# Kernel tuning notes

Measured on AMD Instinct MI355X. Metric: run time of the kernel, lower is better.

Reference implementation:

```python
import jax, jax.numpy as jnp
import numpy as np

RANGE_DISP = 32
IND_INPUT_VIEW = np.array([1, 9]) - 1  # 0-based indices of the two input views
TOTAL_VIEWS = 9                         # an_sparse + an_novel
FEAT_CH = 64


def conv2d(x, w, b):
    # x: (N, Cin, H, W), w: (Cout, Cin, kh, kw), SAME padding, stride 1
    y = jax.lax.conv_general_dilated(x, w, (1, 1), 'SAME',
                                     dimension_numbers=('NCHW', 'OIHW', 'NCHW'))
    return y + b[None, :, None, None]


def unfold_1xK(x, K):
    # torch.nn.functional.unfold(x, kernel_size=(1, K)) for x: (M, C, H, W)
    # -> (M, C, K, H*(W-K+1)), column index = h*(W-K+1) + w (row-major).
    M, C, H, W = x.shape
    out_w = W - K + 1
    cols = jnp.arange(out_w)[None, :] + jnp.arange(K)[:, None]  # (K, out_w)
    y = x[:, :, :, cols]             # (M, C, H, K, out_w)
    y = y.transpose(0, 1, 3, 2, 4)   # (M, C, K, H, out_w)
    return y.reshape(M, C, K, H * out_w)


def setup_inputs() -> dict:
    key = jax.random.key(0)
    ks = jax.random.split(key, 24)
    b, an_sparse, an_novel, rp = 2, 2, 7, 32
    K = RANGE_DISP
    ps = rp + K - 1  # 63

    def rn(k, shape, s=1.0):
        return jax.random.normal(k, shape, dtype=jnp.float32) * s

    W = 0.05  # weight init scale
    return {
        'lf_sparse':        rn(ks[0], (b, an_sparse, rp, ps)),
        'flow_sparse':      rn(ks[1], (b, an_sparse, rp, ps)),
        'warped_lf_sparse': rn(ks[2], (b, an_sparse, rp, ps)),
        'patch_left':       rn(ks[3], (b, an_novel, rp, rp)),
        'patch_right':      rn(ks[4], (b, an_novel, rp, rp)),
        # FlowRefNet: 3 -> 64 -> 64 -> 64, 3x3 convs, SAME
        'fr_w1': rn(ks[5], (FEAT_CH, 3, 3, 3), W), 'fr_b1': jnp.zeros((FEAT_CH,), jnp.float32),
        'fr_w2': rn(ks[6], (FEAT_CH, FEAT_CH, 3, 3), W), 'fr_b2': jnp.zeros((FEAT_CH,), jnp.float32),
        'fr_w3': rn(ks[7], (FEAT_CH, FEAT_CH, 3, 3), W), 'fr_b3': jnp.zeros((FEAT_CH,), jnp.float32),
        # MlpNet: per-disparity MLP 67 -> 64 -> 64 -> 1 (weight head) + conf head 64 -> 1
        'mlp_w1': rn(ks[8], (67, 64), W), 'mlp_b1': jnp.zeros((64,), jnp.float32),
        'mlp_w2': rn(ks[9], (64, 64), W), 'mlp_b2': jnp.zeros((64,), jnp.float32),
        'mlp_w3': rn(ks[10], (64, 1), W), 'mlp_b3': jnp.zeros((1,), jnp.float32),
        'conf_w': rn(ks[11], (64, 1), W), 'conf_b': jnp.zeros((1,), jnp.float32),
        # ViewRefNet: 3 -> 64 -> 64 -> 1 convs, residual on novel patch
        'vr_w1': rn(ks[12], (FEAT_CH, 3, 3, 3), W), 'vr_b1': jnp.zeros((FEAT_CH,), jnp.float32),
        'vr_w2': rn(ks[13], (FEAT_CH, FEAT_CH, 3, 3), W), 'vr_b2': jnp.zeros((FEAT_CH,), jnp.float32),
        'vr_w3': rn(ks[14], (1, FEAT_CH, 3, 3), W), 'vr_b3': jnp.zeros((1,), jnp.float32),
    }


def reference(lf_sparse, flow_sparse, warped_lf_sparse, patch_left, patch_right,
              fr_w1, fr_b1, fr_w2, fr_b2, fr_w3, fr_b3,
              mlp_w1, mlp_b1, mlp_w2, mlp_b2, mlp_w3, mlp_b3, conf_w, conf_b,
              vr_w1, vr_b1, vr_w2, vr_b2, vr_w3, vr_b3):
    b, an_sparse, rp, ps = lf_sparse.shape
    an_novel = patch_left.shape[1]
    K = RANGE_DISP
    N = rp * rp

    lf = lf_sparse.reshape(b * an_sparse, 1, rp, ps)
    fl = flow_sparse.reshape(b * an_sparse, 1, rp, ps)
    wp = warped_lf_sparse.reshape(b * an_sparse, 1, rp, ps)

    # FlowRefNet: flow-feature extraction
    h = jax.nn.relu(conv2d(jnp.concatenate([fl, lf, wp], axis=1), fr_w1, fr_b1))
    h = jax.nn.relu(conv2d(h, fr_w2, fr_b2))
    feat = jax.nn.relu(conv2d(h, fr_w3, fr_b3))  # (b*as, 64, rp, ps)

    # angular code: input-view index minus novel-view index
    ind_novel = np.delete(np.arange(TOTAL_VIEWS), IND_INPUT_VIEW)
    ang = jnp.asarray(IND_INPUT_VIEW[None, :] - ind_novel[:, None], dtype=lf.dtype)  # (an, as)
    spatial = (jnp.arange(K) - K // 2).astype(lf.dtype)  # (K,)

    # EPI windows via unfold(kernel=(1, K))
    flow_unf = unfold_1xK(fl, K)[:, 0]  # (b*as, K, N)
    feat_unf = unfold_1xK(feat, K)      # (b*as, 64, K, N)

    sh = (b, an_novel, an_sparse)
    f_flow = jnp.broadcast_to(flow_unf.reshape(b, 1, an_sparse, 1, K, N),  sh + (1, K, N))
    f_feat = jnp.broadcast_to(feat_unf.reshape(b, 1, an_sparse, FEAT_CH, K, N), sh + (FEAT_CH, K, N))
    f_spat = jnp.broadcast_to(spatial.reshape(1, 1, 1, 1, K, 1),           sh + (1, K, N))
    f_ang  = jnp.broadcast_to(ang.reshape(1, an_novel, an_sparse, 1, 1, 1), sh + (1, K, N))
    features = jnp.concatenate([f_flow, f_feat, f_spat, f_ang], axis=3)  # (b, an, as, 67, K, N)
    # -> (b*an*as*N, K, 67) matching permute(0,3,2,1).reshape in torch
    features = features.transpose(0, 1, 2, 5, 4, 3).reshape(-1, K, 67)

    # MlpNet: per-disparity weight + per-sample confidence
    h1 = jax.nn.relu(features @ mlp_w1 + mlp_b1)
    h2 = jax.nn.relu(h1 @ mlp_w2 + mlp_b2)          # (M2, K, 64)
    weight = (h2 @ mlp_w3 + mlp_b3)[..., 0]         # (M2, K)
    conf = (h2.mean(axis=1) @ conf_w + conf_b)[..., 0]  # (M2,)

    weight = jax.nn.softmax(weight.reshape(b, an_novel, an_sparse, N, K), axis=-1)
    confs = jax.nn.softmax(conf.reshape(b, an_novel, an_sparse, N), axis=2)

    # disparity-weighted combination over EPI windows
    epi = unfold_1xK(lf, K)[:, 0].reshape(b, an_sparse, K, N)
    nv = jnp.einsum('bskn,bvsnk->bvsn', epi, weight)   # (b, an, as, N)
    novel = (nv * confs).sum(axis=2)                   # (b, an, N)

    # ViewRefNet: residual refinement
    pn = novel.reshape(b * an_novel, 1, rp, rp)
    pl = patch_left.reshape(b * an_novel, 1, rp, rp)
    pr = patch_right.reshape(b * an_novel, 1, rp, rp)
    g = jax.nn.relu(conv2d(jnp.concatenate([pn, pl, pr], axis=1), vr_w1, vr_b1))
    g = jax.nn.relu(conv2d(g, vr_w2, vr_b2))
    res = conv2d(g, vr_w3, vr_b3)
    out = pn + res
    return out.reshape(b, an_novel, rp, rp)
```

## Files before the change

kernel.cpp:

```cpp
#include <hip/hip_runtime.h>

typedef unsigned short u16;
typedef unsigned int u32;
typedef __bf16 bf16x8 __attribute__((ext_vector_type(8)));
typedef float f32x4 __attribute__((ext_vector_type(4)));
typedef u16 u16x8 __attribute__((ext_vector_type(8)));

__device__ __forceinline__ u16 f2bf(float f) {
    __bf16 h = (__bf16)f;
    return __builtin_bit_cast(u16, h);
}
__device__ __forceinline__ float bf2f(u16 u) {
    unsigned int x = ((unsigned int)u) << 16;
    return __builtin_bit_cast(float, x);
}

union FragU { u16x8 u; bf16x8 v; };

constexpr size_t WB2F  = 0;
constexpr size_t WB3F  = 18432;
constexpr size_t WBV2  = 36864;
constexpr size_t W1T   = 55296;
constexpr size_t W2T   = 57344;
constexpr size_t X1    = 59392;
constexpr size_t X2    = 317440;
constexpr size_t FEATBF= 575488;
constexpr size_t NOVEL = 833536;
constexpr size_t Y1    = 847872;
constexpr size_t Y2    = 1306624;

__global__ __launch_bounds__(256) void prep_kernel(
    const float* __restrict__ frw2, const float* __restrict__ frw3,
    const float* __restrict__ vrw2,
    const float* __restrict__ mw1, const float* __restrict__ mw2,
    u16* __restrict__ wb2, u16* __restrict__ wb3, u16* __restrict__ wbv,
    u16* __restrict__ w1t, u16* __restrict__ w2t)
{
    const int tid = blockIdx.x * 256 + threadIdx.x;
    const int stride = gridDim.x * 256;
    for (int i = tid; i < 36864; i += stride) {
        int tap = i >> 12, och = (i >> 6) & 63, cin = i & 63;
        size_t s = (size_t)och * 576 + cin * 9 + tap;
        wb2[i] = f2bf(frw2[s]);
        wb3[i] = f2bf(frw3[s]);
        wbv[i] = f2bf(vrw2[s]);
    }
    for (int i = tid; i < 4096; i += stride) {
        int col = i >> 6, r = i & 63;
        w1t[i] = f2bf(mw1[(1 + r) * 64 + col]);
        w2t[i] = f2bf(mw2[r * 64 + col]);
    }
}

template<int W, int NPX>
__global__ __launch_bounds__(256) void conv1_kernel(
    const float* __restrict__ in0, const float* __restrict__ in1,
    const float* __restrict__ in2,
    const float* __restrict__ wts, const float* __restrict__ bias,
    u16* __restrict__ out)
{
    constexpr int H = 32;
    const int t = threadIdx.x;
    const int px = blockIdx.y * 256 + t;
    const int m = blockIdx.z;
    const int og = blockIdx.x;
    if (px >= NPX) return;
    const int y = px / W, x = px - y * W;

    float acc[8];
#pragma unroll
    for (int oc = 0; oc < 8; ++oc) acc[oc] = bias[og * 8 + oc];

#pragma unroll
    for (int cin = 0; cin < 3; ++cin) {
        const float* ip = (cin == 0 ? in0 : (cin == 1 ? in1 : in2)) + (size_t)m * NPX;
        float tap[9];
#pragma unroll
        for (int dy = 0; dy < 3; ++dy) {
            int yy = y + dy - 1;
            bool ry = (yy >= 0) && (yy < H);
#pragma unroll
            for (int dx = 0; dx < 3; ++dx) {
                int xx = x + dx - 1;
                tap[dy * 3 + dx] = (ry && xx >= 0 && xx < W) ? ip[yy * W + xx] : 0.f;
            }
        }
#pragma unroll
        for (int oc = 0; oc < 8; ++oc) {
            const float* wr = wts + (size_t)(og * 8 + oc) * 27 + cin * 9;
#pragma unroll
            for (int j = 0; j < 9; ++j) acc[oc] = fmaf(tap[j], wr[j], acc[oc]);
        }
    }
    u16x8 pk;
#pragma unroll
    for (int oc = 0; oc < 8; ++oc) pk[oc] = f2bf(fmaxf(acc[oc], 0.f));
    *(u16x8*)(out + ((size_t)m * NPX + px) * 64 + og * 8) = pk;
}

template<int W, int NPX>
__global__ __launch_bounds__(256) void convmfma_kernel(
    const u16* __restrict__ in, const u16* __restrict__ wbf,
    const float* __restrict__ bias, u16* __restrict__ out)
{
    constexpr int H = 32;
    const int t = threadIdx.x;
    const int base = blockIdx.x * 64;
    const int m = blockIdx.y;
    const int w = t >> 6, lane = t & 63, q = lane >> 4, l15 = lane & 15;

    const u16* im = in + (size_t)m * NPX * 64;
    const int pxA = base + w * 16 + l15;
    const int yA = pxA / W, xA = pxA - yA * W;
    const bool pxok = (pxA < NPX);

    f32x4 acc[4];
#pragma unroll
    for (int nt = 0; nt < 4; ++nt) acc[nt] = f32x4{0.f, 0.f, 0.f, 0.f};

#pragma unroll
    for (int tap = 0; tap < 9; ++tap) {
        const int dy = tap / 3 - 1, dx = tap % 3 - 1;
        const bool valid = pxok && (yA + dy >= 0) && (yA + dy < H)
                                && (xA + dx >= 0) && (xA + dx < W);
        const u16* ap = im + (size_t)(pxA + dy * W + dx) * 64;
        FragU a0, a1;
        if (valid) {
            a0 = *(const FragU*)(ap + q * 8);
            a1 = *(const FragU*)(ap + 32 + q * 8);
        } else {
#pragma unroll
            for (int jj = 0; jj < 8; ++jj) { a0.u[jj] = 0; a1.u[jj] = 0; }
        }
#pragma unroll
        for (int nt = 0; nt < 4; ++nt) {
            const u16* bp = wbf + tap * 4096 + (nt * 16 + l15) * 64;
            FragU b0 = *(const FragU*)(bp + q * 8);
            FragU b1 = *(const FragU*)(bp + 32 + q * 8);
            acc[nt] = __builtin_amdgcn_mfma_f32_16x16x32_bf16(a0.v, b0.v, acc[nt], 0, 0, 0);
            acc[nt] = __builtin_amdgcn_mfma_f32_16x16x32_bf16(a1.v, b1.v, acc[nt], 0, 0, 0);
        }
    }

#pragma unroll
    for (int nt = 0; nt < 4; ++nt) {
        const float bb = bias[nt * 16 + l15];
#pragma unroll
        for (int e = 0; e < 4; ++e) {
            int pxs = base + w * 16 + q * 4 + e;
            if (pxs < NPX)
                out[((size_t)m * NPX + pxs) * 64 + nt * 16 + l15] =
                    f2bf(fmaxf(acc[nt][e] + bb, 0.f));
        }
    }
}

__global__ __launch_bounds__(256, 2) void mlp_mfma_kernel(
    const float* __restrict__ lf, const float* __restrict__ flow,
    const u16* __restrict__ feat,
    const u16* __restrict__ w1t, const u16* __restrict__ w2t,
    const float* __restrict__ w1, const float* __restrict__ b1,
    const float* __restrict__ b2,
    const float* __restrict__ w3, const float* __restrict__ b3g,
    const float* __restrict__ cw, const float* __restrict__ cbg,
    float* __restrict__ novel)
{
    constexpr int SBS = 72;
    __shared__ __align__(16) float s_vec[7 * 64];
    __shared__ __align__(16) float s_flow[256];
    __shared__ __align__(16) float s_epi[256];
    __shared__ __align__(16) u16 s_base[256 * SBS];
    __shared__ float s_nv[2][7][4];
    __shared__ float s_cf[2][7][4];

    const int t = threadIdx.x;
    const int blk = blockIdx.x;
    const int b = blk >> 7;
    const int n0base = (blk & 127) * 8;
    const int w = t >> 6, lane = t & 63, q = lane >> 4, l15 = lane & 15;
    const int sw = w >> 1;
    const int bsw = b * 2 + sw;

    if (t < 64) {
        s_vec[t]       = b1[t];
        s_vec[64 + t]  = b2[t];
        s_vec[128 + t] = w3[t];
        s_vec[192 + t] = cw[t];
        s_vec[256 + t] = w1[t];
        s_vec[320 + t] = w1[65 * 64 + t];
        s_vec[384 + t] = w1[66 * 64 + t];
    }
    __syncthreads();

    const float b3s = b3g[0];
    const float cbs = cbg[0];

    FragU w1b[2][4];
#pragma unroll
    for (int ks = 0; ks < 2; ++ks)
#pragma unroll
        for (int nt = 0; nt < 4; ++nt)
            w1b[ks][nt] = *(const FragU*)(w1t + (nt * 16 + l15) * 64 + ks * 32 + q * 8);

    FragU w2a[4][2];
#pragma unroll
    for (int mt = 0; mt < 4; ++mt)
#pragma unroll
        for (int ks = 0; ks < 2; ++ks)
            w2a[mt][ks] = *(const FragU*)(w2t + (mt * 16 + l15) * 64 + ks * 32 + q * 8);

    float w1r0pl[4], w1r65pl[4], b1pl[4];
#pragma unroll
    for (int nt = 0; nt < 4; ++nt) {
        int j1 = nt * 16 + l15;
        w1r0pl[nt]  = s_vec[256 + j1];
        w1r65pl[nt] = s_vec[320 + j1];
        b1pl[nt]    = s_vec[j1];
    }
    float w66pl[2][8];
#pragma unroll
    for (int ks = 0; ks < 2; ++ks)
#pragma unroll
        for (int jj = 0; jj < 8; ++jj)
            w66pl[ks][jj] = s_vec[384 + ks * 32 + q * 8 + jj];
    float b2pl[4][4], w3pl[4][4], cwpl[4][4];
#pragma unroll
    for (int mt = 0; mt < 4; ++mt)
#pragma unroll
        for (int e = 0; e < 4; ++e) {
            b2pl[mt][e] = s_vec[64 + mt * 16 + q * 4 + e];
            w3pl[mt][e] = s_vec[128 + mt * 16 + q * 4 + e];
            cwpl[mt][e] = s_vec[192 + mt * 16 + q * 4 + e];
        }

#pragma unroll 1
    for (int iter = 0; iter < 2; ++iter) {
        const int n0 = n0base + iter * 4;
        {
            int ss = t >> 7, nl = (t >> 5) & 3, k = t & 31;
            int n = n0 + nl;
            int a = ((b * 2 + ss) * 32 + (n >> 5)) * 63 + (n & 31) + k;
            s_flow[t] = flow[a];
            s_epi[t]  = lf[a];
        }
        __syncthreads();

#pragma unroll
        for (int mt = 0; mt < 4; ++mt) {
            const int rbase = w * 64 + mt * 16;
            FragU af[2];
            {
                int r = rbase + l15;
                int n = n0 + ((r >> 5) & 3);
                int pos = (n >> 5) * 63 + (n & 31) + (r & 31);
                const u16* fp = feat + ((size_t)bsw * 2016 + pos) * 64;
                af[0] = *(const FragU*)(fp + q * 8);
                af[1] = *(const FragU*)(fp + 32 + q * 8);
            }
            f32x4 flow4 = *(const f32x4*)(s_flow + rbase + q * 4);
#pragma unroll
            for (int nt = 0; nt < 4; ++nt) {
                f32x4 d = {0.f, 0.f, 0.f, 0.f};
                d = __builtin_amdgcn_mfma_f32_16x16x32_bf16(af[0].v, w1b[0][nt].v, d, 0, 0, 0);
                d = __builtin_amdgcn_mfma_f32_16x16x32_bf16(af[1].v, w1b[1][nt].v, d, 0, 0, 0);
#pragma unroll
                for (int e = 0; e < 4; ++e) {
                    int r = rbase + q * 4 + e;
                    int k = r & 31;
                    float val = d[e] + flow4[e] * w1r0pl[nt]
                              + (float)(k - 16) * w1r65pl[nt] + b1pl[nt];
                    s_base[r * SBS + nt * 16 + l15] = f2bf(val);
                }
            }
        }
        __syncthreads();

        float epi_pl[4];
#pragma unroll
        for (int nt = 0; nt < 4; ++nt) epi_pl[nt] = s_epi[w * 64 + nt * 16 + l15];

        for (int v = 0; v < 7; ++v) {
            float ang = (sw == 0) ? -(float)(v + 1) : (float)(7 - v);
            f32x4 acc[4][4];
#pragma unroll
            for (int nt = 0; nt < 4; ++nt) {
                FragU bfr[2];
#pragma unroll
                for (int ks = 0; ks < 2; ++ks) {
                    const u16x8 raw = *(const u16x8*)(s_base + (w * 64 + nt * 16 + l15) * SBS + ks * 32 + q * 8);
#pragma unroll
                    for (int jj = 0; jj < 8; ++jj) {
                        float xv = bf2f(raw[jj]);
                        float hv = fmaxf(xv + ang * w66pl[ks][jj], 0.f);
                        bfr[ks].u[jj] = f2bf(hv);
                    }
                }
#pragma unroll
                for (int mt = 0; mt < 4; ++mt) {
                    f32x4 d = {0.f, 0.f, 0.f, 0.f};
                    d = __builtin_amdgcn_mfma_f32_16x16x32_bf16(w2a[mt][0].v, bfr[0].v, d, 0, 0, 0);
                    d = __builtin_amdgcn_mfma_f32_16x16x32_bf16(w2a[mt][1].v, bfr[1].v, d, 0, 0, 0);
                    acc[mt][nt] = d;
                }
            }
            float wl[4], cfl[4];
#pragma unroll
            for (int nt = 0; nt < 4; ++nt) {
                float wls = 0.f, cfs = 0.f;
#pragma unroll
                for (int mt = 0; mt < 4; ++mt)
#pragma unroll
                    for (int e = 0; e < 4; ++e) {
                        float h2 = fmaxf(acc[mt][nt][e] + b2pl[mt][e], 0.f);
                        wls += h2 * w3pl[mt][e];
                        cfs += h2 * cwpl[mt][e];
                    }
                wls += __shfl_xor(wls, 16); wls += __shfl_xor(wls, 32);
                cfs += __shfl_xor(cfs, 16); cfs += __shfl_xor(cfs, 32);
                wl[nt]  = wls + b3s;
                cfl[nt] = cfs;
            }
#pragma unroll
            for (int ni = 0; ni < 2; ++ni) {
                float a0 = wl[ni * 2], a1 = wl[ni * 2 + 1];
                float mx = fmaxf(a0, a1);
#pragma unroll
                for (int msk = 1; msk <= 8; msk <<= 1) mx = fmaxf(mx, __shfl_xor(mx, msk));
                float e0 = __expf(a0 - mx), e1 = __expf(a1 - mx);
                float ssum = e0 + e1;
                float nvp = e0 * epi_pl[ni * 2] + e1 * epi_pl[ni * 2 + 1];
                float cfp = cfl[ni * 2] + cfl[ni * 2 + 1];
#pragma unroll
                for (int msk = 1; msk <= 8; msk <<= 1) {
                    ssum += __shfl_xor(ssum, msk);
                    nvp  += __shfl_xor(nvp, msk);
                    cfp  += __shfl_xor(cfp, msk);
                }
                if (lane == 0) {
                    int nloc = (w & 1) * 2 + ni;
                    s_nv[sw][v][nloc] = nvp / ssum;
                    s_cf[sw][v][nloc] = cfp * (1.f / 32.f) + cbs;
                }
            }
        }
        __syncthreads();

        if (t < 28) {
            int v = t >> 2, nl = t & 3;
            float c0 = s_cf[0][v][nl], c1 = s_cf[1][v][nl];
            float mx = fmaxf(c0, c1);
            float e0 = __expf(c0 - mx), e1 = __expf(c1 - mx);
            novel[(size_t)(b * 7 + v) * 1024 + n0 + nl] =
                (e0 * s_nv[0][v][nl] + e1 * s_nv[1][v][nl]) / (e0 + e1);
        }
    }
}

__global__ __launch_bounds__(256) void convlast_kernel(
    const u16* __restrict__ in,
    const float* __restrict__ wts,
    const float* __restrict__ bias,
    const float* __restrict__ resid,
    float* __restrict__ out)
{
    __shared__ float sw3[576];
    const int t = threadIdx.x;
    for (int i = t; i < 576; i += 256) sw3[i] = wts[i];
    __syncthreads();

    const int tid = blockIdx.x * 256 + t;
    const int m = tid >> 10, p = tid & 1023;
    const int y = p >> 5, x = p & 31;
    float a = bias[0] + resid[tid];
    const u16* im = in + ((size_t)m * 1024 + p) * 64;
#pragma unroll
    for (int dy = 0; dy < 3; ++dy) {
        int yy = y + dy - 1;
        if (yy < 0 || yy >= 32) continue;
#pragma unroll
        for (int dx = 0; dx < 3; ++dx) {
            int xx = x + dx - 1;
            if (xx < 0 || xx >= 32) continue;
            const u16* ip = im + (size_t)((dy - 1) * 32 + (dx - 1)) * 64;
            const int tap = dy * 3 + dx;
#pragma unroll
            for (int cg = 0; cg < 8; ++cg) {
                u16x8 raw = *(const u16x8*)(ip + cg * 8);
#pragma unroll
                for (int e = 0; e < 8; ++e)
                    a = fmaf(bf2f(raw[e]), sw3[(cg * 8 + e) * 9 + tap], a);
            }
        }
    }
    out[tid] = a;
}

extern "C" void kernel_launch(void* const* d_in, const int* in_sizes, int n_in,
                              void* d_out, int out_size, void* d_ws, size_t ws_size,
                              hipStream_t stream) {
    const float* lf   = (const float*)d_in[0];
    const float* flow = (const float*)d_in[1];
    const float* wp   = (const float*)d_in[2];
    const float* pl   = (const float*)d_in[3];
    const float* pr   = (const float*)d_in[4];
    float* ws = (float*)d_ws;

    prep_kernel<<<128, 256, 0, stream>>>(
        (const float*)d_in[7], (const float*)d_in[9], (const float*)d_in[21],
        (const float*)d_in[11], (const float*)d_in[13],
        (u16*)(ws + WB2F), (u16*)(ws + WB3F), (u16*)(ws + WBV2),
        (u16*)(ws + W1T), (u16*)(ws + W2T));

    conv1_kernel<63, 2016><<<dim3(8, 8, 4), 256, 0, stream>>>(
        flow, lf, wp, (const float*)d_in[5], (const float*)d_in[6],
        (u16*)(ws + X1));
    convmfma_kernel<63, 2016><<<dim3(32, 4), 256, 0, stream>>>(
        (const u16*)(ws + X1), (const u16*)(ws + WB2F), (const float*)d_in[8],
        (u16*)(ws + X2));
    convmfma_kernel<63, 2016><<<dim3(32, 4), 256, 0, stream>>>(
        (const u16*)(ws + X2), (const u16*)(ws + WB3F), (const float*)d_in[10],
        (u16*)(ws + FEATBF));

    mlp_mfma_kernel<<<256, 256, 0, stream>>>(
        lf, flow, (const u16*)(ws + FEATBF),
        (const u16*)(ws + W1T), (const u16*)(ws + W2T),
        (const float*)d_in[11], (const float*)d_in[12],
        (const float*)d_in[14],
        (const float*)d_in[15], (const float*)d_in[16],
        (const float*)d_in[17], (const float*)d_in[18],
        ws + NOVEL);

    conv1_kernel<32, 1024><<<dim3(8, 4, 14), 256, 0, stream>>>(
        ws + NOVEL, pl, pr, (const float*)d_in[19], (const float*)d_in[20],
        (u16*)(ws + Y1));
    convmfma_kernel<32, 1024><<<dim3(16, 14), 256, 0, stream>>>(
        (const u16*)(ws + Y1), (const u16*)(ws + WBV2), (const float*)d_in[22],
        (u16*)(ws + Y2));
    convlast_kernel<<<56, 256, 0, stream>>>(
        (const u16*)(ws + Y2), (const float*)d_in[23], (const float*)d_in[24],
        ws + NOVEL, (float*)d_out);
}
```

Baseline: 218.5 us.

## Split MLP kernel across sparse views and add separate confidence-combine kernel

The MLP kernel previously had each block handle both sparse views and iterate twice over 4-position chunks, combining confidence softmax in shared memory. Now each block handles one sparse view and 8 positions in a single pass, doubling the grid to 512 blocks. It writes per-view weighted values and confidences to workspace, and a new small combine kernel applies the 2-way softmax. This raises parallelism and removes the serial iteration loop, at the cost of an extra launch and global round-trip for intermediate results.

```diff
diff --git a/kernel.cpp b/kernel.cpp
--- a/kernel.cpp
+++ b/kernel.cpp
@@ -25,9 +25,11 @@
 constexpr size_t X1    = 59392;
 constexpr size_t X2    = 317440;
 constexpr size_t FEATBF= 575488;
-constexpr size_t NOVEL = 833536;
-constexpr size_t Y1    = 847872;
-constexpr size_t Y2    = 1306624;
+constexpr size_t NVOFF = 833536;
+constexpr size_t CFOFF = 862208;
+constexpr size_t NOVEL = 890880;
+constexpr size_t Y1    = 905216;
+constexpr size_t Y2    = 1363968;
 
 __global__ __launch_bounds__(256) void prep_kernel(
     const float* __restrict__ frw2, const float* __restrict__ frw3,
@@ -163,23 +165,20 @@
     const float* __restrict__ b2,
     const float* __restrict__ w3, const float* __restrict__ b3g,
     const float* __restrict__ cw, const float* __restrict__ cbg,
-    float* __restrict__ novel)
+    float* __restrict__ nv_out, float* __restrict__ cf_out)
 {
     constexpr int SBS = 72;
     __shared__ __align__(16) float s_vec[7 * 64];
     __shared__ __align__(16) float s_flow[256];
     __shared__ __align__(16) float s_epi[256];
     __shared__ __align__(16) u16 s_base[256 * SBS];
-    __shared__ float s_nv[2][7][4];
-    __shared__ float s_cf[2][7][4];
 
     const int t = threadIdx.x;
     const int blk = blockIdx.x;
-    const int b = blk >> 7;
-    const int n0base = (blk & 127) * 8;
+    const int bs = blk >> 7;
+    const int n0 = (blk & 127) * 8;
+    const int b = bs >> 1, s = bs & 1;
     const int w = t >> 6, lane = t & 63, q = lane >> 4, l15 = lane & 15;
-    const int sw = w >> 1;
-    const int bsw = b * 2 + sw;
 
     if (t < 64) {
         s_vec[t]       = b1[t];
@@ -190,6 +189,13 @@
         s_vec[320 + t] = w1[65 * 64 + t];
         s_vec[384 + t] = w1[66 * 64 + t];
     }
+    {
+        int nl = t >> 5, k = t & 31;
+        int n = n0 + nl;
+        int a = (bs * 32 + (n >> 5)) * 63 + (n & 31) + k;
+        s_flow[t] = flow[a];
+        s_epi[t]  = lf[a];
+    }
     __syncthreads();
 
     const float b3s = b3g[0];
@@ -201,13 +207,6 @@
 #pragma unroll
         for (int nt = 0; nt < 4; ++nt)
             w1b[ks][nt] = *(const FragU*)(w1t + (nt * 16 + l15) * 64 + ks * 32 + q * 8);
-
-    FragU w2a[4][2];
-#pragma unroll
-    for (int mt = 0; mt < 4; ++mt)
-#pragma unroll
-        for (int ks = 0; ks < 2; ++ks)
-            w2a[mt][ks] = *(const FragU*)(w2t + (mt * 16 + l15) * 64 + ks * 32 + q * 8);
 
     float w1r0pl[4], w1r65pl[4], b1pl[4];
 #pragma unroll
@@ -217,12 +216,51 @@
         w1r65pl[nt] = s_vec[320 + j1];
         b1pl[nt]    = s_vec[j1];
     }
+
+#pragma unroll
+    for (int mt = 0; mt < 4; ++mt) {
+        const int rbase = w * 64 + mt * 16;
+        FragU af[2];
+        {
+            int r = rbase + l15;
+            int n = n0 + (r >> 5);
+            int pos = (n >> 5) * 63 + (n & 31) + (r & 31);
+            const u16* fp = feat + ((size_t)bs * 2016 + pos) * 64;
+            af[0] = *(const FragU*)(fp + q * 8);
+            af[1] = *(const FragU*)(fp + 32 + q * 8);
+        }
+        f32x4 flow4 = *(const f32x4*)(s_flow + rbase + q * 4);
+#pragma unroll
+        for (int nt = 0; nt < 4; ++nt) {
+            f32x4 d = {0.f, 0.f, 0.f, 0.f};
+            d = __builtin_amdgcn_mfma_f32_16x16x32_bf16(af[0].v, w1b[0][nt].v, d, 0, 0, 0);
+            d = __builtin_amdgcn_mfma_f32_16x16x32_bf16(af[1].v, w1b[1][nt].v, d, 0, 0, 0);
+#pragma unroll
+            for (int e = 0; e < 4; ++e) {
+                int r = rbase + q * 4 + e;
+                int k = r & 31;
+                float val = d[e] + flow4[e] * w1r0pl[nt]
+                          + (float)(k - 16) * w1r65pl[nt] + b1pl[nt];
+                s_base[r * SBS + nt * 16 + l15] = f2bf(val);
+            }
+        }
+    }
+    __syncthreads();
+
+    FragU w2a[4][2];
+#pragma unroll
+    for (int mt = 0; mt < 4; ++mt)
+#pragma unroll
+        for (int ks = 0; ks < 2; ++ks)
+            w2a[mt][ks] = *(const FragU*)(w2t + (mt * 16 + l15) * 64 + ks * 32 + q * 8);
+
     float w66pl[2][8];
 #pragma unroll
     for (int ks = 0; ks < 2; ++ks)
 #pragma unroll
         for (int jj = 0; jj < 8; ++jj)
             w66pl[ks][jj] = s_vec[384 + ks * 32 + q * 8 + jj];
+
     float b2pl[4][4], w3pl[4][4], cwpl[4][4];
 #pragma unroll
     for (int mt = 0; mt < 4; ++mt)
@@ -232,128 +270,89 @@
             w3pl[mt][e] = s_vec[128 + mt * 16 + q * 4 + e];
             cwpl[mt][e] = s_vec[192 + mt * 16 + q * 4 + e];
         }
-
-#pragma unroll 1
-    for (int iter = 0; iter < 2; ++iter) {
-        const int n0 = n0base + iter * 4;
-        {
-            int ss = t >> 7, nl = (t >> 5) & 3, k = t & 31;
-            int n = n0 + nl;
-            int a = ((b * 2 + ss) * 32 + (n >> 5)) * 63 + (n & 31) + k;
-            s_flow[t] = flow[a];
-            s_epi[t]  = lf[a];
-        }
-        __syncthreads();
-
-#pragma unroll
-        for (int mt = 0; mt < 4; ++mt) {
-            const int rbase = w * 64 + mt * 16;
-            FragU af[2];
-            {
-                int r = rbase + l15;
-                int n = n0 + ((r >> 5) & 3);
-                int pos = (n >> 5) * 63 + (n & 31) + (r & 31);
-                const u16* fp = feat + ((size_t)bsw * 2016 + pos) * 64;
-                af[0] = *(const FragU*)(fp + q * 8);
-                af[1] = *(const FragU*)(fp + 32 + q * 8);
-            }
-            f32x4 flow4 = *(const f32x4*)(s_flow + rbase + q * 4);
-#pragma unroll
-            for (int nt = 0; nt < 4; ++nt) {
+    float epi_pl[4];
+#pragma unroll
+    for (int nt = 0; nt < 4; ++nt) epi_pl[nt] = s_epi[w * 64 + nt * 16 + l15];
+
+    for (int v = 0; v < 7; ++v) {
+        float ang = (s == 0) ? -(float)(v + 1) : (float)(7 - v);
+        f32x4 acc[4][4];
+#pragma unroll
+        for (int nt = 0; nt < 4; ++nt) {
+            FragU bfr[2];
+#pragma unroll
+            for (int ks = 0; ks < 2; ++ks) {
+                const u16x8 raw = *(const u16x8*)(s_base + (w * 64 + nt * 16 + l15) * SBS + ks * 32 + q * 8);
+#pragma unroll
+                for (int jj = 0; jj < 8; ++jj) {
+                    float xv = bf2f(raw[jj]);
+                    float hv = fmaxf(xv + ang * w66pl[ks][jj], 0.f);
+                    bfr[ks].u[jj] = f2bf(hv);
+                }
+            }
+#pragma unroll
+            for (int mt = 0; mt < 4; ++mt) {
                 f32x4 d = {0.f, 0.f, 0.f, 0.f};
-                d = __builtin_amdgcn_mfma_f32_16x16x32_bf16(af[0].v, w1b[0][nt].v, d, 0, 0, 0);
-                d = __builtin_amdgcn_mfma_f32_16x16x32_bf16(af[1].v, w1b[1][nt].v, d, 0, 0, 0);
+                d = __builtin_amdgcn_mfma_f32_16x16x32_bf16(w2a[mt][0].v, bfr[0].v, d, 0, 0, 0);
+                d = __builtin_amdgcn_mfma_f32_16x16x32_bf16(w2a[mt][1].v, bfr[1].v, d, 0, 0, 0);
+                acc[mt][nt] = d;
+            }
+        }
+        float wl[4], cfl[4];
+#pragma unroll
+        for (int nt = 0; nt < 4; ++nt) {
+            float wls = 0.f, cfs = 0.f;
+#pragma unroll
+            for (int mt = 0; mt < 4; ++mt)
 #pragma unroll
                 for (int e = 0; e < 4; ++e) {
-                    int r = rbase + q * 4 + e;
-                    int k = r & 31;
-                    float val = d[e] + flow4[e] * w1r0pl[nt]
-                              + (float)(k - 16) * w1r65pl[nt] + b1pl[nt];
-                    s_base[r * SBS + nt * 16 + l15] = f2bf(val);
+                    float h2 = fmaxf(acc[mt][nt][e] + b2pl[mt][e], 0.f);
+                    wls += h2 * w3pl[mt][e];
+                    cfs += h2 * cwpl[mt][e];
                 }
-            }
-        }
-        __syncthreads();
-
-        float epi_pl[4];
-#pragma unroll
-        for (int nt = 0; nt < 4; ++nt) epi_pl[nt] = s_epi[w * 64 + nt * 16 + l15];
-
-        for (int v = 0; v < 7; ++v) {
-            float ang = (sw == 0) ? -(float)(v + 1) : (float)(7 - v);
-            f32x4 acc[4][4];
-#pragma unroll
-            for (int nt = 0; nt < 4; ++nt) {
-                FragU bfr[2];
-#pragma unroll
-                for (int ks = 0; ks < 2; ++ks) {
-                    const u16x8 raw = *(const u16x8*)(s_base + (w * 64 + nt * 16 + l15) * SBS + ks * 32 + q * 8);
-#pragma unroll
-                    for (int jj = 0; jj < 8; ++jj) {
-                        float xv = bf2f(raw[jj]);
-                        float hv = fmaxf(xv + ang * w66pl[ks][jj], 0.f);
-                        bfr[ks].u[jj] = f2bf(hv);
-                    }
-                }
-#pragma unroll
-                for (int mt = 0; mt < 4; ++mt) {
-                    f32x4 d = {0.f, 0.f, 0.f, 0.f};
-                    d = __builtin_amdgcn_mfma_f32_16x16x32_bf16(w2a[mt][0].v, bfr[0].v, d, 0, 0, 0);
-                    d = __builtin_amdgcn_mfma_f32_16x16x32_bf16(w2a[mt][1].v, bfr[1].v, d, 0, 0, 0);
-                    acc[mt][nt] = d;
-                }
-            }
-            float wl[4], cfl[4];
-#pragma unroll
-            for (int nt = 0; nt < 4; ++nt) {
-                float wls = 0.f, cfs = 0.f;
-#pragma unroll
-                for (int mt = 0; mt < 4; ++mt)
-#pragma unroll
-                    for (int e = 0; e < 4; ++e) {
-                        float h2 = fmaxf(acc[mt][nt][e] + b2pl[mt][e], 0.f);
-                        wls += h2 * w3pl[mt][e];
-                        cfs += h2 * cwpl[mt][e];
-                    }
-                wls += __shfl_xor(wls, 16); wls += __shfl_xor(wls, 32);
-                cfs += __shfl_xor(cfs, 16); cfs += __shfl_xor(cfs, 32);
-                wl[nt]  = wls + b3s;
-                cfl[nt] = cfs;
-            }
-#pragma unroll
-            for (int ni = 0; ni < 2; ++ni) {
-                float a0 = wl[ni * 2], a1 = wl[ni * 2 + 1];
-                float mx = fmaxf(a0, a1);
-#pragma unroll
-                for (int msk = 1; msk <= 8; msk <<= 1) mx = fmaxf(mx, __shfl_xor(mx, msk));
-                float e0 = __expf(a0 - mx), e1 = __expf(a1 - mx);
-                float ssum = e0 + e1;
-                float nvp = e0 * epi_pl[ni * 2] + e1 * epi_pl[ni * 2 + 1];
-                float cfp = cfl[ni * 2] + cfl[ni * 2 + 1];
-#pragma unroll
-                for (int msk = 1; msk <= 8; msk <<= 1) {
-                    ssum += __shfl_xor(ssum, msk);
-                    nvp  += __shfl_xor(nvp, msk);
-                    cfp  += __shfl_xor(cfp, msk);
-                }
-                if (lane == 0) {
-                    int nloc = (w & 1) * 2 + ni;
-                    s_nv[sw][v][nloc] = nvp / ssum;
-                    s_cf[sw][v][nloc] = cfp * (1.f / 32.f) + cbs;
-                }
-            }
-        }
-        __syncthreads();
-
-        if (t < 28) {
-            int v = t >> 2, nl = t & 3;
-            float c0 = s_cf[0][v][nl], c1 = s_cf[1][v][nl];
-            float mx = fmaxf(c0, c1);
-            float e0 = __expf(c0 - mx), e1 = __expf(c1 - mx);
-            novel[(size_t)(b * 7 + v) * 1024 + n0 + nl] =
-                (e0 * s_nv[0][v][nl] + e1 * s_nv[1][v][nl]) / (e0 + e1);
-        }
-    }
+            wls += __shfl_xor(wls, 16); wls += __shfl_xor(wls, 32);
+            cfs += __shfl_xor(cfs, 16); cfs += __shfl_xor(cfs, 32);
+            wl[nt]  = wls + b3s;
+            cfl[nt] = cfs;
+        }
+#pragma unroll
+        for (int ni = 0; ni < 2; ++ni) {
+            float a0 = wl[ni * 2], a1 = wl[ni * 2 + 1];
+            float mx = fmaxf(a0, a1);
+#pragma unroll
+            for (int msk = 1; msk <= 8; msk <<= 1) mx = fmaxf(mx, __shfl_xor(mx, msk));
+            float e0 = __expf(a0 - mx), e1 = __expf(a1 - mx);
+            float ssum = e0 + e1;
+            float nvp = e0 * epi_pl[ni * 2] + e1 * epi_pl[ni * 2 + 1];
+            float cfp = cfl[ni * 2] + cfl[ni * 2 + 1];
+#pragma unroll
+            for (int msk = 1; msk <= 8; msk <<= 1) {
+                ssum += __shfl_xor(ssum, msk);
+                nvp  += __shfl_xor(nvp, msk);
+                cfp  += __shfl_xor(cfp, msk);
+            }
+            if (lane == 0) {
+                int n = n0 + w * 2 + ni;
+                size_t idx = ((size_t)(b * 7 + v) * 2 + s) * 1024 + n;
+                nv_out[idx] = nvp / ssum;
+                cf_out[idx] = cfp * (1.f / 32.f) + cbs;
+            }
+        }
+    }
+}
+
+__global__ void combine_kernel(const float* __restrict__ nv, const float* __restrict__ cf,
+                               float* __restrict__ novel) {
+    int tid = blockIdx.x * 256 + threadIdx.x;
+    if (tid >= 2 * 7 * 1024) return;
+    int n = tid & 1023;
+    int bv = tid >> 10;
+    size_t i0 = ((size_t)bv * 2 + 0) * 1024 + n;
+    size_t i1 = ((size_t)bv * 2 + 1) * 1024 + n;
+    float c0 = cf[i0], c1 = cf[i1];
+    float mx = fmaxf(c0, c1);
+    float e0 = __expf(c0 - mx), e1 = __expf(c1 - mx);
+    novel[tid] = (e0 * nv[i0] + e1 * nv[i1]) / (e0 + e1);
 }
 
 __global__ __launch_bounds__(256) void convlast_kernel(
@@ -421,14 +420,16 @@
         (const u16*)(ws + X2), (const u16*)(ws + WB3F), (const float*)d_in[10],
         (u16*)(ws + FEATBF));
 
-    mlp_mfma_kernel<<<256, 256, 0, stream>>>(
+    mlp_mfma_kernel<<<512, 256, 0, stream>>>(
         lf, flow, (const u16*)(ws + FEATBF),
         (const u16*)(ws + W1T), (const u16*)(ws + W2T),
         (const float*)d_in[11], (const float*)d_in[12],
         (const float*)d_in[14],
         (const float*)d_in[15], (const float*)d_in[16],
         (const float*)d_in[17], (const float*)d_in[18],
-        ws + NOVEL);
+        ws + NVOFF, ws + CFOFF);
+
+    combine_kernel<<<56, 256, 0, stream>>>(ws + NVOFF, ws + CFOFF, ws + NOVEL);
 
     conv1_kernel<32, 1024><<<dim3(8, 4, 14), 256, 0, stream>>>(
         ws + NOVEL, pl, pr, (const float*)d_in[19], (const float*)d_in[20],
```

Result: faster. 195.8 us (-10.4%).
